# Kernel optimization log

Hardware: AMD Instinct MI355X
Metric: run time of the kernel (lower is better)

Reference implementation:

```python
import jax, jax.numpy as jnp
import numpy as np
import math
from jax import lax

# Resampler constants (match Sampler(orig_freq=16000, new_freq=24000) with
# torchaudio-kaldi defaults: lowpass_filter_width=6, cutoff=0.99*0.5*min_freq)
ORIG = 16000
NEW = 24000
LPF_WIDTH = 6


def _filters():
    """Static polyphase windowed-sinc filter bank (numpy, trace-time).

    Returns (first_indices[int], weights[P, W] float32, in_unit, out_unit).
    Faithful to Sampler._get_LR_indices_and_weights.
    """
    base = math.gcd(ORIG, NEW)
    in_unit = ORIG // base          # conv stride
    out_unit = NEW // base          # number of phases
    cutoff = 0.99 * 0.5 * min(ORIG, NEW)
    ww = LPF_WIDTH / (2.0 * cutoff)  # window half-width in seconds
    out_t = np.arange(out_unit, dtype=np.float64) / NEW
    min_idx = np.ceil((out_t - ww) * ORIG)
    max_idx = np.floor((out_t + ww) * ORIG)
    W = int((max_idx - min_idx + 1).max())  # max filter width (taps)
    j = np.arange(W)[None, :]
    inp_idx = min_idx[:, None] + j
    dt = inp_idx / ORIG - out_t[:, None]     # [P, W] delta times
    w = np.zeros_like(dt)
    inside = np.abs(dt) < ww
    w[inside] = 0.5 * (1.0 + np.cos(2.0 * math.pi * cutoff / LPF_WIDTH * dt[inside]))
    nz = dt != 0.0
    w[nz] *= np.sin(2.0 * math.pi * cutoff * dt[nz]) / (math.pi * dt[nz])
    w[~nz] *= 2.0 * cutoff
    w /= ORIG
    return min_idx.astype(np.int64), w.astype(np.float32), in_unit, out_unit


def _num_output_samples(L):
    """Sampler._get_num_LR_output_samples (Kaldi GetNumOutputSamples)."""
    tick_freq = ORIG * NEW // math.gcd(ORIG, NEW)
    interval = L * (tick_freq // ORIG)
    ticks_per_out = tick_freq // NEW
    last = interval // ticks_per_out
    if last * ticks_per_out == interval:
        last -= 1
    return last + 1


def setup_inputs() -> dict:
    key = jax.random.key(0)
    waveform = jax.random.normal(key, (8, 4_000_000), dtype=jnp.float32)
    _, w, _, _ = _filters()
    return {"waveform": waveform, "weights": jnp.asarray(w)}


def reference(waveform, weights):
    first_indices, _, in_unit, out_unit = _filters()  # static ints
    C, L = waveform.shape
    W = weights.shape[1]
    tot = _num_output_samples(L)
    max_unit_index = (tot - 1) // out_unit
    end_index_of_last_window = max_unit_index * in_unit + W
    out = jnp.zeros((C, tot), dtype=waveform.dtype)
    dn = ("NCH", "OIH", "NCH")  # channels act as batch (groups=C equivalent)
    for i in range(out_unit):  # small fixed phase count (3)
        f = int(first_indices[i])
        left_pad = max(0, -f)
        start = max(0, f)
        right_pad = max(0, end_index_of_last_window + 1 - (L - f))
        wav = jnp.pad(waveform[:, start:], ((0, 0), (left_pad, right_pad)))
        # strided valid FIR: [C, 1, len] * [1, 1, W] -> [C, 1, U]
        conv = lax.conv_general_dilated(
            wav[:, None, :], weights[i][None, None, :],
            window_strides=(in_unit,), padding="VALID",
            dimension_numbers=dn)[:, 0, :]
        U = conv.shape[1]
        # phase i writes output positions i, i+out_unit, ... (disjoint phases)
        pos = i + out_unit * jnp.arange(U)
        valid = pos < tot
        out = out.at[:, jnp.minimum(pos, tot - 1)].add(
            jnp.where(valid[None, :], conv, jnp.zeros((), conv.dtype)))
    return out
```

## Files before the change

### kernel.cpp

```cpp
#include <hip/hip_runtime.h>
#include <hip/hip_bf16.h>
#include <math.h>


#define NCH   8
#define TAPS  13
#define BLOCK 256

struct Taps {
    float w[3][TAPS];
};

__global__ __launch_bounds__(BLOCK) void resample_kernel(
    const float* __restrict__ x,
    float* __restrict__ out,
    Taps wt,
    int L, int tot, int U)
{
    __shared__ float sx[2 * BLOCK + 16];

    const int tid = threadIdx.x;
    const int c   = blockIdx.y;
    const int u0  = blockIdx.x * BLOCK;
    const long g0 = 2L * u0 - 6;
    const float* xc = x + (long)c * L;

    for (int s = tid; s < 2 * BLOCK + 15; s += BLOCK) {
        long idx = g0 + s;
        sx[s] = (idx >= 0 && idx < (long)L) ? xc[idx] : 0.0f;
    }
    __syncthreads();

    const int u = u0 + tid;
    if (u >= U) return;

    float win[16];
    const float2* sx2 = (const float2*)&sx[2 * tid];
#pragma unroll
    for (int k = 0; k < 8; ++k) {
        float2 v = sx2[k];
        win[2 * k]     = v.x;
        win[2 * k + 1] = v.y;
    }

    float acc0 = 0.f, acc1 = 0.f, acc2 = 0.f;
#pragma unroll
    for (int j = 0; j < TAPS; ++j) {
        acc0 = fmaf(wt.w[0][j], win[j],     acc0);
        acc1 = fmaf(wt.w[1][j], win[j + 1], acc1);
        acc2 = fmaf(wt.w[2][j], win[j + 2], acc2);
    }

    const long t0 = 3L * u;
    float* oc = out + (long)c * tot;
    oc[t0] = acc0;
    if (t0 + 1 < tot) oc[t0 + 1] = acc1;
    if (t0 + 2 < tot) oc[t0 + 2] = acc2;
}

static void compute_weights(Taps* t) {
    const double ORIG = 16000.0, NEWF = 24000.0, LPFW = 6.0;
    const double cutoff = 0.99 * 0.5 * ORIG;
    const double ww = LPFW / (2.0 * cutoff);
    for (int p = 0; p < 3; ++p) {
        double out_t = (double)p / NEWF;
        double min_idx = ceil((out_t - ww) * ORIG);
        for (int j = 0; j < TAPS; ++j) {
            double inp = min_idx + (double)j;
            double dt = inp / ORIG - out_t;
            double w = 0.0;
            if (fabs(dt) < ww)
                w = 0.5 * (1.0 + cos(2.0 * M_PI * cutoff / LPFW * dt));
            if (dt != 0.0)
                w *= sin(2.0 * M_PI * cutoff * dt) / (M_PI * dt);
            else
                w *= 2.0 * cutoff;
            w /= ORIG;
            t->w[p][j] = (float)w;
        }
    }
}

extern "C" void kernel_launch(void* const* d_in, const int* in_sizes, int n_in,
                              void* d_out, int out_size, void* d_ws, size_t ws_size,
                              hipStream_t stream) {
    const float* x = (const float*)d_in[0];
    float* out     = (float*)d_out;

    const int L   = in_sizes[0] / NCH;
    const int tot = out_size / NCH;
    const int U   = (tot + 2) / 3;

    Taps wt;
    compute_weights(&wt);

    dim3 grid((U + BLOCK - 1) / BLOCK, NCH);
    resample_kernel<<<grid, BLOCK, 0, stream>>>(x, out, wt, L, tot, U);
}
```

Before: 314.0 us.

## Compute twelve outputs per thread with float4 input loads and stores

Each thread now produces four polyphase units (12 outputs) instead of one, staging input through shared memory with float4 loads and writing results as three float4 stores. This targets the scalar, stride-3 global stores and the per-thread overhead of the memory-bound resampler. The trade-off is more registers per thread and four times fewer blocks, and the float4 stores depend on the alignment of each channel's output row (tot*c).

```diff
diff --git a/kernel.cpp b/kernel.cpp
--- a/kernel.cpp
+++ b/kernel.cpp
@@ -6,56 +6,82 @@
 #define NCH   8
 #define TAPS  13
 #define BLOCK 256
+#define OUTS_PER_THREAD 12
+#define U_PER_BLOCK     (4 * BLOCK)
+#define SX_FLOATS       (8 * BLOCK + 24)
+#define SX_UNITS        (SX_FLOATS / 4)
 
-struct Taps {
-    float w[3][TAPS];
-};
+struct Taps { float w[3][TAPS]; };
 
 __global__ __launch_bounds__(BLOCK) void resample_kernel(
     const float* __restrict__ x,
     float* __restrict__ out,
     Taps wt,
-    int L, int tot, int U)
+    int L, int tot)
 {
-    __shared__ float sx[2 * BLOCK + 16];
+    __shared__ float sx[SX_FLOATS + 8];
 
-    const int tid = threadIdx.x;
-    const int c   = blockIdx.y;
-    const int u0  = blockIdx.x * BLOCK;
-    const long g0 = 2L * u0 - 6;
+    const int lt = threadIdx.x;
+    const int c  = blockIdx.y;
+    const long base = 2048L * blockIdx.x - 8;
     const float* xc = x + (long)c * L;
 
-    for (int s = tid; s < 2 * BLOCK + 15; s += BLOCK) {
-        long idx = g0 + s;
-        sx[s] = (idx >= 0 && idx < (long)L) ? xc[idx] : 0.0f;
+    for (int s = lt; s < SX_UNITS; s += BLOCK) {
+        long idx4 = base + 4L * s;
+        float4 v;
+        if (idx4 >= 0 && idx4 + 4 <= L) {
+            v = *(const float4*)(xc + idx4);
+        } else {
+            float t[4];
+#pragma unroll
+            for (int j = 0; j < 4; ++j) {
+                long idx = idx4 + j;
+                t[j] = (idx >= 0 && idx < (long)L) ? xc[idx] : 0.0f;
+            }
+            v = make_float4(t[0], t[1], t[2], t[3]);
+        }
+        ((float4*)sx)[s] = v;
     }
     __syncthreads();
 
-    const int u = u0 + tid;
-    if (u >= U) return;
+    const long gt = (long)blockIdx.x * BLOCK + lt;
+    const long n0 = OUTS_PER_THREAD * gt;
+    if (n0 >= tot) return;
 
-    float win[16];
-    const float2* sx2 = (const float2*)&sx[2 * tid];
+    float win[24];
+    const float4* sx4 = (const float4*)&sx[8 * lt];
 #pragma unroll
-    for (int k = 0; k < 8; ++k) {
-        float2 v = sx2[k];
-        win[2 * k]     = v.x;
-        win[2 * k + 1] = v.y;
+    for (int k = 0; k < 6; ++k) {
+        float4 v = sx4[k];
+        win[4 * k]     = v.x;
+        win[4 * k + 1] = v.y;
+        win[4 * k + 2] = v.z;
+        win[4 * k + 3] = v.w;
     }
 
-    float acc0 = 0.f, acc1 = 0.f, acc2 = 0.f;
+    float acc[4][3];
 #pragma unroll
-    for (int j = 0; j < TAPS; ++j) {
-        acc0 = fmaf(wt.w[0][j], win[j],     acc0);
-        acc1 = fmaf(wt.w[1][j], win[j + 1], acc1);
-        acc2 = fmaf(wt.w[2][j], win[j + 2], acc2);
+    for (int j = 0; j < 4; ++j)
+#pragma unroll
+        for (int p = 0; p < 3; ++p) {
+            float a = 0.f;
+#pragma unroll
+            for (int t = 0; t < TAPS; ++t)
+                a = fmaf(wt.w[p][t], win[2 * j + p + 2 + t], a);
+            acc[j][p] = a;
+        }
+
+    float* oc = out + (long)c * tot;
+    if (n0 + OUTS_PER_THREAD <= tot) {
+        float4* o4 = (float4*)(oc + n0);
+        o4[0] = make_float4(acc[0][0], acc[0][1], acc[0][2], acc[1][0]);
+        o4[1] = make_float4(acc[1][1], acc[1][2], acc[2][0], acc[2][1]);
+        o4[2] = make_float4(acc[2][2], acc[3][0], acc[3][1], acc[3][2]);
+    } else {
+#pragma unroll
+        for (int k = 0; k < OUTS_PER_THREAD; ++k)
+            if (n0 + k < tot) oc[n0 + k] = acc[k / 3][k % 3];
     }
-
-    const long t0 = 3L * u;
-    float* oc = out + (long)c * tot;
-    oc[t0] = acc0;
-    if (t0 + 1 < tot) oc[t0 + 1] = acc1;
-    if (t0 + 2 < tot) oc[t0 + 2] = acc2;
 }
 
 static void compute_weights(Taps* t) {
@@ -89,11 +115,11 @@
 
     const int L   = in_sizes[0] / NCH;
     const int tot = out_size / NCH;
-    const int U   = (tot + 2) / 3;
 
     Taps wt;
     compute_weights(&wt);
 
-    dim3 grid((U + BLOCK - 1) / BLOCK, NCH);
-    resample_kernel<<<grid, BLOCK, 0, stream>>>(x, out, wt, L, tot, U);
+    const int outs_per_block = BLOCK * OUTS_PER_THREAD;
+    dim3 grid((tot + outs_per_block - 1) / outs_per_block, NCH);
+    resample_kernel<<<grid, BLOCK, 0, stream>>>(x, out, wt, L, tot);
 }
```

Result: faster. 287.4 us (-8.5%).
